# Performance work log

Hardware: AMD Instinct MI355X
Metric: run time of the kernel (lower is better)

Reference implementation:

```python
import jax, jax.numpy as jnp
import numpy as np

B, T, N, F = 16, 12, 1024, 8
H = 64        # hidden_size
K = 2         # diffusion order (DCRNN k == DiffConv gnn_kernel)
HORIZON = 12
E = 32 * N    # number of edges


def setup_inputs() -> dict:
    key = jax.random.key(0)
    ks = jax.random.split(key, 16)
    s = 0.05
    inp = {}
    inp['x'] = jax.random.normal(ks[0], (B, T, N, F), jnp.float32)
    inp['edge_index'] = jax.random.randint(ks[1], (2, E), 0, N)
    inp['edge_weight'] = jax.random.uniform(ks[2], (E,), jnp.float32)
    inp['adj'] = jax.random.uniform(ks[3], (N, N), jnp.float32)
    # encoder Linear(F -> H)
    inp['W_enc'] = jax.random.normal(ks[4], (F, H), jnp.float32) * s
    inp['b_enc'] = jnp.zeros((H,), jnp.float32)
    # NodeEmbedding(n_nodes, H)
    inp['node_emb'] = jax.random.normal(ks[5], (N, H), jnp.float32) * s
    # DCRNN gates: DenseGraphConvOrderK(2H -> H), 2 supports x K hops (include_self=False)
    gin = 2 * H * 2 * K
    inp['W_r'] = jax.random.normal(ks[6], (gin, H), jnp.float32) * s
    inp['b_r'] = jnp.zeros((H,), jnp.float32)
    inp['W_u'] = jax.random.normal(ks[7], (gin, H), jnp.float32) * s
    inp['b_u'] = jnp.zeros((H,), jnp.float32)
    inp['W_c'] = jax.random.normal(ks[8], (gin, H), jnp.float32) * s
    inp['b_c'] = jnp.zeros((H,), jnp.float32)
    # DiffConv filters: Linear(H*(2K+1) -> H), root_weight=True, add_backward=True
    din = H * (2 * K + 1)
    inp['W_diff'] = jax.random.normal(ks[9], (din, H), jnp.float32) * s
    inp['b_diff'] = jnp.zeros((H,), jnp.float32)
    # decoder Linear(H -> F*HORIZON)
    inp['W_dec'] = jax.random.normal(ks[10], (H, F * HORIZON), jnp.float32) * s
    inp['b_dec'] = jnp.zeros((F * HORIZON,), jnp.float32)
    return inp


def _dgconv(x, supports, W, b):
    # DenseGraphConvOrderK, include_self=False: for each support, K hop powers, concat on channels.
    feats = []
    for a in supports:  # a: [n, n], row-normalized transition matrix
        x1 = x
        for _ in range(K):
            x1 = jnp.einsum('bvc,wv->bwc', x1, a)
            feats.append(x1)
    return jnp.concatenate(feats, axis=-1) @ W + b


def _forward(x, edge_index, edge_weight, adj, W_enc, b_enc, node_emb,
             W_r, b_r, W_u, b_u, W_c, b_c, W_diff, b_diff, W_dec, b_dec):
    # --- DenseGraphConvOrderK.compute_support: fwd/bwd row-normalized transitions ---
    adj_fwd = adj / adj.sum(1, keepdims=True)
    adjT = adj.T
    adj_bwd = adjT / adjT.sum(1, keepdims=True)
    supports = (adj_fwd, adj_bwd)

    # encoder + node embeddings (broadcast over batch & time)
    x_enc = x @ W_enc + b_enc + node_emb  # [B, T, N, H]

    # --- DenseDCRNN: GRU with diffusion-conv gates, scan over time ---
    def step(h, xt):
        xh = jnp.concatenate([xt, h], axis=-1)                 # [B, N, 2H]
        r = jax.nn.sigmoid(_dgconv(xh, supports, W_r, b_r))    # forget/reset gate
        u = jax.nn.sigmoid(_dgconv(xh, supports, W_u, b_u))    # update gate
        xc = jnp.concatenate([xt, r * h], axis=-1)
        c = jnp.tanh(_dgconv(xc, supports, W_c, b_c))          # candidate
        h_new = u * h + (1.0 - u) * c
        return h_new, None

    h0 = jnp.zeros((B, N, H), x_enc.dtype)
    h, _ = jax.lax.scan(step, h0, jnp.swapaxes(x_enc, 0, 1))   # last state, [B, N, H]

    # --- DiffConv readout on sparse edge list (root + K fwd hops + K bwd hops) ---
    src, dst = edge_index[0], edge_index[1]

    def norm_w(group_idx):
        deg = jax.ops.segment_sum(edge_weight, group_idx, num_segments=N)
        inv = jnp.where(deg > 0, 1.0 / deg, 0.0)
        return edge_weight * inv[group_idx]

    w_fwd = norm_w(dst)  # normalize over target (dim=1)
    w_bwd = norm_w(src)  # flipped edges, normalized over their targets (= src)

    feats = [h]
    for s_, d_, w_ in ((src, dst, w_fwd), (dst, src, w_bwd)):
        xs = h
        for _ in range(K):
            msg = xs[:, s_, :] * w_[None, :, None]             # [B, E, H]
            xs = jnp.zeros_like(h).at[:, d_, :].add(msg)
            feats.append(xs)
    z = jnp.concatenate(feats, axis=-1) @ W_diff + b_diff      # [B, N, H]

    # decoder + rearrange 'b n (t f) -> b t n f'
    out = z @ W_dec + b_dec                                    # [B, N, HORIZON*F]
    return out.reshape(B, N, HORIZON, F).transpose(0, 2, 1, 3) # [B, HORIZON, N, F]


def reference(x, edge_index, edge_weight, adj, W_enc, b_enc, node_emb,
              W_r, b_r, W_u, b_u, W_c, b_c, W_diff, b_diff, W_dec, b_dec):
    return _forward(x, edge_index, edge_weight, adj, W_enc, b_enc, node_emb,
                    W_r, b_r, W_u, b_u, W_c, b_c, W_diff, b_diff, W_dec, b_dec)
```

## Files before the change

### kernel.cpp

```cpp
#include <hip/hip_runtime.h>
#include <math.h>

#define BB 16
#define TT 12
#define NN 1024
#define FF 8
#define HH 64
#define EE 32768
#define DIN 320
#define ODIM 96
#define APAD 40

typedef _Float16 v8h __attribute__((ext_vector_type(8)));
typedef float v4f __attribute__((ext_vector_type(4)));

__device__ __forceinline__ unsigned short f2h(float v) {
    _Float16 h = (_Float16)v;
    unsigned short u;
    __builtin_memcpy(&u, &h, 2);
    return u;
}
__device__ __forceinline__ float h2f(unsigned short u) {
    _Float16 h;
    __builtin_memcpy(&h, &u, 2);
    return (float)h;
}
__device__ __forceinline__ void gl_lds16(const void* g, void* l) {
    __builtin_amdgcn_global_load_lds(
        (const __attribute__((address_space(1))) unsigned int*)g,
        (__attribute__((address_space(3))) unsigned int*)l, 16, 0, 0);
}

__global__ void k_ei_detect(const int* __restrict__ ei_raw, int* __restrict__ flag) {
    __shared__ int s[256];
    s[threadIdx.x] = ei_raw[2 * threadIdx.x + 1];
    __syncthreads();
    for (int st = 128; st > 0; st >>= 1) {
        if (threadIdx.x < st) s[threadIdx.x] |= s[threadIdx.x + st];
        __syncthreads();
    }
    if (threadIdx.x == 0) flag[0] = (s[0] == 0) ? 1 : 0;
}
__global__ void k_ei_norm(const int* __restrict__ ei_raw, const int* __restrict__ flag,
                          int* __restrict__ ei32) {
    int j = blockIdx.x * 256 + threadIdx.x;
    ei32[j] = flag[0] ? ei_raw[2 * j] : ei_raw[j];
}

__global__ void k_rowsum(const float* __restrict__ adj, float* __restrict__ rinv) {
    __shared__ float s[256];
    int i = blockIdx.x;
    float acc = 0.f;
    for (int j = threadIdx.x; j < NN; j += 256) acc += adj[i * NN + j];
    s[threadIdx.x] = acc;
    __syncthreads();
    for (int st = 128; st > 0; st >>= 1) {
        if (threadIdx.x < st) s[threadIdx.x] += s[threadIdx.x + st];
        __syncthreads();
    }
    if (threadIdx.x == 0) rinv[i] = (s[0] != 0.f) ? 1.f / s[0] : 0.f;
}
__global__ void k_colsumP(const float* __restrict__ adj, float* __restrict__ csum) {
    int bi = blockIdx.x;
    int j4 = threadIdx.x * 4;
    float4 acc = {0.f, 0.f, 0.f, 0.f};
    const float* base = adj + (size_t)bi * 16 * NN + j4;
    #pragma unroll
    for (int r = 0; r < 16; r++) {
        float4 v = *(const float4*)(base + (size_t)r * NN);
        acc.x += v.x; acc.y += v.y; acc.z += v.z; acc.w += v.w;
    }
    atomicAdd(&csum[j4 + 0], acc.x);
    atomicAdd(&csum[j4 + 1], acc.y);
    atomicAdd(&csum[j4 + 2], acc.z);
    atomicAdd(&csum[j4 + 3], acc.w);
}
__global__ void k_cinv(const float* __restrict__ csum, float* __restrict__ cinv) {
    int j = blockIdx.x * 256 + threadIdx.x;
    float s = csum[j];
    cinv[j] = (s != 0.f) ? 1.f / s : 0.f;
}

__global__ __launch_bounds__(256) void k_prepA(
        const float* __restrict__ adj, const float* __restrict__ rinv,
        const float* __restrict__ cinv, unsigned short* __restrict__ Mp) {
    int w0 = blockIdx.x * 64, v0 = blockIdx.y * 64;
    __shared__ float T[64][68];
    int row = threadIdx.x >> 2, cs = (threadIdx.x & 3) * 16;
    #pragma unroll
    for (int j = 0; j < 4; j++)
        *(float4*)&T[row][cs + j * 4] = *(const float4*)(adj + (size_t)(w0 + row) * NN + v0 + cs + j * 4);
    __syncthreads();
    {
        float sc = rinv[w0 + row];
        unsigned short h8[16];
        #pragma unroll
        for (int j = 0; j < 16; j++) h8[j] = f2h(T[row][cs + j] * sc);
        size_t ofs = (size_t)(w0 + row) * NN + v0 + cs;
        ((uint4*)(Mp + ofs))[0] = *(uint4*)&h8[0];
        ((uint4*)(Mp + ofs))[1] = *(uint4*)&h8[8];
    }
    {
        float sc = cinv[v0 + row];
        unsigned short h8[16];
        #pragma unroll
        for (int j = 0; j < 16; j++) h8[j] = f2h(T[cs + j][row] * sc);
        size_t ofs = (size_t)2048 * NN + (size_t)(v0 + row) * NN + w0 + cs;
        ((uint4*)(Mp + ofs))[0] = *(uint4*)&h8[0];
        ((uint4*)(Mp + ofs))[1] = *(uint4*)&h8[8];
    }
}

__global__ __launch_bounds__(256) void k_msq(unsigned short* __restrict__ M) {
    int zz = blockIdx.z;
    size_t srcb = (size_t)zz * 2048 * NN;
    size_t dstb = srcb + (size_t)1024 * NN;
    int w0 = blockIdx.x * 64, n0 = blockIdx.y * 64;

    __shared__ unsigned short sA[64 * APAD];
    __shared__ unsigned short sB[64 * APAD];

    int tid = threadIdx.x;
    int lane = tid & 63, wave = tid >> 6;
    int wr = (wave >> 1) * 32, wc = (wave & 1) * 32;
    int l15 = lane & 15, quad = lane >> 4;
    int arow = tid >> 2, akk = (tid & 3) * 8;
    int bkr = tid & 31, bc8 = (tid >> 5) * 8;

    v4f acc[2][2];
    #pragma unroll
    for (int i = 0; i < 2; i++)
        #pragma unroll
        for (int j = 0; j < 2; j++) { acc[i][j][0]=0.f; acc[i][j][1]=0.f; acc[i][j][2]=0.f; acc[i][j][3]=0.f; }

    for (int k0 = 0; k0 < NN; k0 += 32) {
        *(uint4*)&sA[arow * APAD + akk] = *(const uint4*)(M + srcb + (size_t)(w0 + arow) * NN + k0 + akk);
        uint4 bh = *(const uint4*)(M + srcb + (size_t)(k0 + bkr) * NN + n0 + bc8);
        const unsigned short* ph = (const unsigned short*)&bh;
        #pragma unroll
        for (int j = 0; j < 8; j++) sB[(bc8 + j) * APAD + bkr] = ph[j];
        __syncthreads();

        v8h a0 = *(const v8h*)&sA[(wr + l15) * APAD + quad * 8];
        v8h a1 = *(const v8h*)&sA[(wr + 16 + l15) * APAD + quad * 8];
        #pragma unroll
        for (int j = 0; j < 2; j++) {
            v8h bb = *(const v8h*)&sB[(wc + j * 16 + l15) * APAD + quad * 8];
            acc[0][j] = __builtin_amdgcn_mfma_f32_16x16x32_f16(a0, bb, acc[0][j], 0, 0, 0);
            acc[1][j] = __builtin_amdgcn_mfma_f32_16x16x32_f16(a1, bb, acc[1][j], 0, 0, 0);
        }
        __syncthreads();
    }

    #pragma unroll
    for (int i = 0; i < 2; i++)
        #pragma unroll
        for (int j = 0; j < 2; j++) {
            int rb = w0 + wr + i * 16 + quad * 4;
            int cc = n0 + wc + j * 16 + l15;
            #pragma unroll
            for (int rr = 0; rr < 4; rr++)
                M[dstb + (size_t)(rb + rr) * NN + cc] = f2h(acc[i][j][rr]);
        }
}

__global__ void k_m2frag(const unsigned short* __restrict__ P, unsigned short* __restrict__ F) {
    size_t t = (size_t)blockIdx.x * 256 + threadIdx.x;
    int rowloc = (int)(t & 63);
    int kc = (int)((t >> 6) & 127);
    int T = (int)(t >> 13);
    size_t src = ((size_t)(T * 64 + rowloc) * NN) + kc * 8;
    *(uint4*)(F + t * 8) = *(const uint4*)(P + src);
}

__global__ void k_xT(const float* __restrict__ x, unsigned short* __restrict__ XallT) {
    int bx = blockIdx.x;
    int t = bx >> 4, b = bx & 15;
    int tid = threadIdx.x;
    int f = tid & 7, half = tid >> 3;
    const float* xs = x + ((size_t)b * TT + t) * NN * FF + f;
    int n0 = half * 32;
    unsigned short v[32];
    #pragma unroll
    for (int i = 0; i < 32; i++) v[i] = f2h(xs[(size_t)(n0 + i) * FF]);
    unsigned short* dst = XallT + ((size_t)bx * 8 + f) * NN + n0;
    #pragma unroll
    for (int i = 0; i < 4; i++) *(uint4*)(dst + i * 8) = *(uint4*)&v[i * 8];
}
__global__ void k_embT(const float* __restrict__ emb, unsigned short* __restrict__ XallT) {
    int c = blockIdx.x;
    int n0 = threadIdx.x * 4;
    unsigned short v[4];
    #pragma unroll
    for (int j = 0; j < 4; j++) v[j] = f2h(emb[(size_t)(n0 + j) * HH + c]);
    *(uint2*)(XallT + (size_t)(1536 + c) * NN + n0) = *(uint2*)v;
}

__global__ __launch_bounds__(512) void k_hopX(
        const unsigned short* __restrict__ Mf,
        const unsigned short* __restrict__ XallT,
        unsigned short* __restrict__ AX, unsigned short* __restrict__ Eg) {
    int bid = blockIdx.x;
    int rt = bid & 31;
    int y  = bid >> 5;
    int g = rt >> 3;
    int n0 = (rt & 7) * 128;
    int c0 = y * 128;

    __shared__ unsigned short sA[2][16 * 512];
    __shared__ unsigned short sX[2][16 * 512];

    int tid = threadIdx.x;
    int lane = tid & 63, wave = tid >> 6;
    int rh = wave >> 2, cq = wave & 3;
    int l15 = lane & 15, quad = lane >> 4;

    v4f acc[4][2];
    #pragma unroll
    for (int i = 0; i < 4; i++)
        #pragma unroll
        for (int j = 0; j < 2; j++) { acc[i][j][0]=0.f; acc[i][j][1]=0.f; acc[i][j][2]=0.f; acc[i][j][3]=0.f; }

    auto STAGE = [&](int buf, int k0) {
        #pragma unroll
        for (int s = 0; s < 4; s++) {
            int id = wave + s * 8;
            if (id < 16) {
                int ah = id >> 3, kh = (id >> 2) & 1, rf = id & 3;
                const unsigned short* src = Mf +
                    ((size_t)(rt * 2 + ah) * 8192 +
                     (size_t)((k0 >> 3) + kh * 4 + quad) * 64 + rf * 16 + l15) * 8;
                gl_lds16(src, &sA[buf][id * 512]);
            } else {
                int xi = id - 16, cj = xi >> 1, kh = xi & 1;
                const unsigned short* src = XallT +
                    (size_t)(c0 + cj * 16 + l15) * NN + k0 + kh * 32 + quad * 8;
                gl_lds16(src, &sX[buf][xi * 512]);
            }
        }
    };

    STAGE(0, 0);
    STAGE(1, 64);

    int lu = lane * 8;
    for (int kt = 0; kt < 16; kt++) {
        int cur = kt & 1;
        if (kt < 15) asm volatile("s_waitcnt vmcnt(4)" ::: "memory");
        else         asm volatile("s_waitcnt vmcnt(0)" ::: "memory");
        __builtin_amdgcn_s_barrier();
        asm volatile("" ::: "memory");
        #pragma unroll
        for (int kh = 0; kh < 2; kh++) {
            v8h a[4], bx[2];
            #pragma unroll
            for (int rf = 0; rf < 4; rf++)
                a[rf] = *(const v8h*)&sA[cur][(rh * 8 + kh * 4 + rf) * 512 + lu];
            #pragma unroll
            for (int j = 0; j < 2; j++)
                bx[j] = *(const v8h*)&sX[cur][((cq * 2 + j) * 2 + kh) * 512 + lu];
            #pragma unroll
            for (int rf = 0; rf < 4; rf++)
                #pragma unroll
                for (int j = 0; j < 2; j++)
                    acc[rf][j] = __builtin_amdgcn_mfma_f32_16x16x32_f16(a[rf], bx[j], acc[rf][j], 0, 0, 0);
        }
        asm volatile("" ::: "memory");
        __builtin_amdgcn_s_barrier();
        asm volatile("" ::: "memory");
        if (kt < 14) STAGE(cur, (kt + 2) * 64);
    }

    #pragma unroll
    for (int rf = 0; rf < 4; rf++)
        #pragma unroll
        for (int j = 0; j < 2; j++) {
            int col = c0 + cq * 32 + j * 16 + l15;
            #pragma unroll
            for (int rr = 0; rr < 4; rr++) {
                int nrow = n0 + rh * 64 + rf * 16 + quad * 4 + rr;
                if (col < 1536) {
                    int tb = col >> 3, f = col & 7;
                    AX[((size_t)tb * NN + nrow) * 32 + g * 8 + f] = f2h(acc[rf][j][rr]);
                } else if (col < 1600) {
                    int cc = col - 1536;
                    Eg[((size_t)(g << 10) + nrow) * 64 + cc] = f2h(acc[rf][j][rr]);
                }
            }
        }
}

__global__ void k_veg(const float* __restrict__ W_enc,
                      const float* __restrict__ W_r, const float* __restrict__ W_u,
                      const float* __restrict__ W_c, float* __restrict__ Veg) {
    int idx = blockIdx.x * 256 + threadIdx.x;
    int c = idx & 63;
    int gf = (idx >> 6) & 31;
    int G = idx >> 11;
    int g = gf >> 3, f = gf & 7;
    const float* W = (G == 0) ? W_r : ((G == 1) ? W_u : W_c);
    float acc = 0.f;
    for (int c2 = 0; c2 < 64; c2++)
        acc += W_enc[f * HH + c2] * W[(size_t)(g * 128 + c2) * HH + c];
    Veg[idx] = acc;
}

__global__ void k_constE(const unsigned short* __restrict__ Eg, const float* __restrict__ b_enc,
                         const float* __restrict__ W_r, const float* __restrict__ W_u,
                         const float* __restrict__ W_c, float* __restrict__ constE) {
    int G = blockIdx.y;
    int n = blockIdx.x * 4 + (threadIdx.x >> 6);
    int c = threadIdx.x & 63;
    const float* W = (G == 0) ? W_r : ((G == 1) ? W_u : W_c);
    float acc = 0.f;
    for (int g = 0; g < 4; g++)
        for (int c2 = 0; c2 < 64; c2++)
            acc += (h2f(Eg[((size_t)(g << 10) + n) * 64 + c2]) + b_enc[c2]) *
                   W[(size_t)(g * 128 + c2) * HH + c];
    constE[((size_t)G << 16) + (size_t)n * 64 + c] = acc;
}

__global__ void k_wfragH(const float* __restrict__ W_r, const float* __restrict__ W_u,
                         const float* __restrict__ W_c,
                         unsigned short* __restrict__ Fr, unsigned short* __restrict__ Fu,
                         unsigned short* __restrict__ Fc) {
    int idx = blockIdx.x * 256 + threadIdx.x;
    int G = idx >> 14;
    int r = idx & 16383;
    int e = r & 7, l = (r >> 3) & 63;
    int rest = r >> 9;
    int ks = rest & 7, cj = rest >> 3;
    int c = cj * 16 + (l & 15);
    int k = ks * 32 + (l >> 4) * 8 + e;
    int g = k >> 6, c2 = k & 63;
    const float* W = (G == 0) ? W_r : ((G == 1) ? W_u : W_c);
    unsigned short* F = (G == 0) ? Fr : ((G == 1) ? Fu : Fc);
    F[r] = f2h(W[(size_t)(g * 128 + 64 + c2) * HH + c]);
}
__global__ void k_wfragX(const float* __restrict__ Veg, unsigned short* __restrict__ Wx) {
    int idx = blockIdx.x * 256 + threadIdx.x;
    int G = idx >> 11;
    int r = idx & 2047;
    int e = r & 7, l = (r >> 3) & 63;
    int cj = r >> 9;
    int c = cj * 16 + (l & 15);
    int k = (l >> 4) * 8 + e;
    Wx[idx] = f2h(Veg[(size_t)G * 2048 + (size_t)k * 64 + c]);
}

__global__ void k_wfragO(const float* __restrict__ W_diff, const float* __restrict__ W_dec,
                         unsigned short* __restrict__ Wf) {
    int idx = blockIdx.x * 256 + threadIdx.x;
    int e = idx & 7, l = (idx >> 3) & 63;
    int rest = idx >> 9;
    int ks = rest % 10, cj = rest / 10;
    int o = cj * 16 + (l & 15);
    int k = ks * 32 + (l >> 4) * 8 + e;
    float acc = 0.f;
    for (int c = 0; c < 64; c++) acc += W_diff[(size_t)k * HH + c] * W_dec[(size_t)c * ODIM + o];
    Wf[idx] = f2h(acc);
}
__global__ void k_bzd(const float* __restrict__ b_diff, const float* __restrict__ W_dec,
                      const float* __restrict__ b_dec, float* __restrict__ bzd) {
    int o = threadIdx.x;
    float acc = b_dec[o];
    for (int c = 0; c < 64; c++) acc += b_diff[c] * W_dec[(size_t)c * ODIM + o];
    bzd[o] = acc;
}

__global__ __launch_bounds__(512) void k_hopRU(
        const unsigned short* __restrict__ Mf,
        const unsigned short* __restrict__ XhH,
        const unsigned short* __restrict__ AXt,
        const unsigned short* __restrict__ WfrH, const unsigned short* __restrict__ WfuH,
        const unsigned short* __restrict__ Wxr, const unsigned short* __restrict__ Wxu,
        const float* __restrict__ b_r, const float* __restrict__ b_u,
        const float* __restrict__ constE,
        const float* __restrict__ h,
        unsigned short* __restrict__ XhR, float* __restrict__ ubuf) {
    int bid = blockIdx.x;
    int b = bid >> 5, nth = bid & 31;
    int nt = nth >> 1, hb = nth & 1;
    int n0 = nth * 32;

    __shared__ unsigned short S[2][24 * 512];

    int tid = threadIdx.x;
    int lane = tid & 63, wave = tid >> 6;
    int l15 = lane & 15, quad = lane >> 4;
    int g = wave >> 1, rh = wave & 1;

    const unsigned short* Xbase = XhH + (size_t)b * 64 * NN;

    v4f acc[4];
    #pragma unroll
    for (int j = 0; j < 4; j++) { acc[j][0]=0.f; acc[j][1]=0.f; acc[j][2]=0.f; acc[j][3]=0.f; }

    auto STAGE = [&](int buf, int k0) {
        #pragma unroll
        for (int s = 0; s < 3; s++) {
            int id = wave + s * 8;
            if (id < 16) {
                int gg = id >> 2, kh = (id >> 1) & 1, rfi = id & 1;
                int rf = hb * 2 + rfi;
                const unsigned short* src = Mf +
                    ((size_t)(gg * 16 + nt) * 8192 +
                     (size_t)((k0 >> 3) + kh * 4 + quad) * 64 + rf * 16 + l15) * 8;
                gl_lds16(src, &S[buf][id * 512]);
            } else {
                int xi = id - 16, cj = xi >> 1, kh = xi & 1;
                const unsigned short* src = Xbase +
                    (size_t)(cj * 16 + l15) * NN + k0 + kh * 32 + quad * 8;
                gl_lds16(src, &S[buf][id * 512]);
            }
        }
    };

    STAGE(0, 0);
    STAGE(1, 64);

    int lu = lane * 8;
    for (int kt = 0; kt < 16; kt++) {
        int cur = kt & 1;
        if (kt < 15) asm volatile("s_waitcnt vmcnt(3)" ::: "memory");
        else         asm volatile("s_waitcnt vmcnt(0)" ::: "memory");
        __builtin_amdgcn_s_barrier();
        asm volatile("" ::: "memory");
        #pragma unroll
        for (int kh = 0; kh < 2; kh++) {
            v8h a = *(const v8h*)&S[cur][(g * 4 + kh * 2 + rh) * 512 + lu];
            #pragma unroll
            for (int cj = 0; cj < 4; cj++) {
                v8h bx = *(const v8h*)&S[cur][(16 + cj * 2 + kh) * 512 + lu];
                acc[cj] = __builtin_amdgcn_mfma_f32_16x16x32_f16(a, bx, acc[cj], 0, 0, 0);
            }
        }
        asm volatile("" ::: "memory");
        __builtin_amdgcn_s_barrier();
        asm volatile("" ::: "memory");
        if (kt < 14) STAGE(cur, (kt + 2) * 64);
    }

    unsigned short* Yt = &S[0][0];
    #pragma unroll
    for (int cj = 0; cj < 4; cj++) {
        int col = g * 64 + cj * 16 + l15;
        #pragma unroll
        for (int rr = 0; rr < 4; rr++) {
            int row = rh * 16 + quad * 4 + rr;
            Yt[row * 264 + col] = f2h(acc[cj][rr]);
        }
    }
    __syncthreads();

    int gate = wave >> 2, rw = (wave >> 1) & 1, ch = wave & 1;
    const unsigned short* WH = gate ? WfuH : WfrH;
    const unsigned short* WX = gate ? Wxu : Wxr;
    const float* bias = gate ? b_u : b_r;
    const float* cE = constE + ((size_t)gate << 16);

    v4f acc2[2];
    #pragma unroll
    for (int j = 0; j < 2; j++) { acc2[j][0]=0.f; acc2[j][1]=0.f; acc2[j][2]=0.f; acc2[j][3]=0.f; }

    {
        v8h ax = *(const v8h*)(AXt + ((size_t)(b << 10) + n0 + rw * 16 + l15) * 32 + quad * 8);
        #pragma unroll
        for (int j = 0; j < 2; j++) {
            v8h bf = *(const v8h*)(WX + (size_t)(ch * 2 + j) * 512 + lu);
            acc2[j] = __builtin_amdgcn_mfma_f32_16x16x32_f16(ax, bf, acc2[j], 0, 0, 0);
        }
    }
    #pragma unroll
    for (int ks = 0; ks < 8; ks++) {
        v8h a = *(const v8h*)&Yt[(rw * 16 + l15) * 264 + ks * 32 + quad * 8];
        #pragma unroll
        for (int j = 0; j < 2; j++) {
            v8h bf = *(const v8h*)(WH + (size_t)((ch * 2 + j) * 8 + ks) * 512 + lu);
            acc2[j] = __builtin_amdgcn_mfma_f32_16x16x32_f16(a, bf, acc2[j], 0, 0, 0);
        }
    }

    unsigned short* sT = &S[1][0];
    if (gate == 0) {
        #pragma unroll
        for (int j = 0; j < 2; j++) {
            int c = (ch * 2 + j) * 16 + l15;
            float bb = bias[c];
            #pragma unroll
            for (int rr = 0; rr < 4; rr++) {
                int nl = rw * 16 + quad * 4 + rr;
                size_t row = (size_t)(b << 10) + n0 + nl;
                float pre = acc2[j][rr] + bb + cE[(size_t)(n0 + nl) * 64 + c];
                float r = 1.f / (1.f + expf(-pre));
                sT[c * 36 + nl] = f2h(r * h[row * 64 + c]);
            }
        }
    } else {
        #pragma unroll
        for (int j = 0; j < 2; j++) {
            int c = (ch * 2 + j) * 16 + l15;
            float bb = bias[c];
            #pragma unroll
            for (int rr = 0; rr < 4; rr++) {
                int nl = rw * 16 + quad * 4 + rr;
                size_t row = (size_t)(b << 10) + n0 + nl;
                float pre = acc2[j][rr] + bb + cE[(size_t)(n0 + nl) * 64 + c];
                ubuf[row * 64 + c] = 1.f / (1.f + expf(-pre));
            }
        }
    }
    __syncthreads();
    {
        int c = tid >> 3, n4 = (tid & 7) * 4;
        *(uint2*)(XhR + ((size_t)b * 64 + c) * NN + n0 + n4) = *(uint2*)&sT[c * 36 + n4];
    }
}

__global__ __launch_bounds__(512) void k_hopC(
        const unsigned short* __restrict__ Mf,
        const unsigned short* __restrict__ XhR,
        const unsigned short* __restrict__ AXt,
        const unsigned short* __restrict__ WfcH, const unsigned short* __restrict__ Wxc,
        const float* __restrict__ b_c,
        const float* __restrict__ constE,
        const float* __restrict__ ubuf,
        float* __restrict__ h, unsigned short* __restrict__ XhH) {
    int bid = blockIdx.x;
    int b = bid >> 5, nth = bid & 31;
    int nt = nth >> 1, hb = nth & 1;
    int n0 = nth * 32;

    __shared__ unsigned short S[2][24 * 512];

    int tid = threadIdx.x;
    int lane = tid & 63, wave = tid >> 6;
    int l15 = lane & 15, quad = lane >> 4;
    int g = wave >> 1, rh = wave & 1;

    const unsigned short* Xbase = XhR + (size_t)b * 64 * NN;

    v4f acc[4];
    #pragma unroll
    for (int j = 0; j < 4; j++) { acc[j][0]=0.f; acc[j][1]=0.f; acc[j][2]=0.f; acc[j][3]=0.f; }

    auto STAGE = [&](int buf, int k0) {
        #pragma unroll
        for (int s = 0; s < 3; s++) {
            int id = wave + s * 8;
            if (id < 16) {
                int gg = id >> 2, kh = (id >> 1) & 1, rfi = id & 1;
                int rf = hb * 2 + rfi;
                const unsigned short* src = Mf +
                    ((size_t)(gg * 16 + nt) * 8192 +
                     (size_t)((k0 >> 3) + kh * 4 + quad) * 64 + rf * 16 + l15) * 8;
                gl_lds16(src, &S[buf][id * 512]);
            } else {
                int xi = id - 16, cj = xi >> 1, kh = xi & 1;
                const unsigned short* src = Xbase +
                    (size_t)(cj * 16 + l15) * NN + k0 + kh * 32 + quad * 8;
                gl_lds16(src, &S[buf][id * 512]);
            }
        }
    };

    STAGE(0, 0);
    STAGE(1, 64);

    int lu = lane * 8;
    for (int kt = 0; kt < 16; kt++) {
        int cur = kt & 1;
        if (kt < 15) asm volatile("s_waitcnt vmcnt(3)" ::: "memory");
        else         asm volatile("s_waitcnt vmcnt(0)" ::: "memory");
        __builtin_amdgcn_s_barrier();
        asm volatile("" ::: "memory");
        #pragma unroll
        for (int kh = 0; kh < 2; kh++) {
            v8h a = *(const v8h*)&S[cur][(g * 4 + kh * 2 + rh) * 512 + lu];
            #pragma unroll
            for (int cj = 0; cj < 4; cj++) {
                v8h bx = *(const v8h*)&S[cur][(16 + cj * 2 + kh) * 512 + lu];
                acc[cj] = __builtin_amdgcn_mfma_f32_16x16x32_f16(a, bx, acc[cj], 0, 0, 0);
            }
        }
        asm volatile("" ::: "memory");
        __builtin_amdgcn_s_barrier();
        asm volatile("" ::: "memory");
        if (kt < 14) STAGE(cur, (kt + 2) * 64);
    }

    unsigned short* Yt = &S[0][0];
    #pragma unroll
    for (int cj = 0; cj < 4; cj++) {
        int col = g * 64 + cj * 16 + l15;
        #pragma unroll
        for (int rr = 0; rr < 4; rr++) {
            int row = rh * 16 + quad * 4 + rr;
            Yt[row * 264 + col] = f2h(acc[cj][rr]);
        }
    }
    __syncthreads();

    int ch = wave >> 1, rw = wave & 1;
    const float* cE = constE + ((size_t)2 << 16);

    v4f acc2;
    acc2[0]=0.f; acc2[1]=0.f; acc2[2]=0.f; acc2[3]=0.f;

    {
        v8h ax = *(const v8h*)(AXt + ((size_t)(b << 10) + n0 + rw * 16 + l15) * 32 + quad * 8);
        v8h bf = *(const v8h*)(Wxc + (size_t)ch * 512 + lu);
        acc2 = __builtin_amdgcn_mfma_f32_16x16x32_f16(ax, bf, acc2, 0, 0, 0);
    }
    #pragma unroll
    for (int ks = 0; ks < 8; ks++) {
        v8h a = *(const v8h*)&Yt[(rw * 16 + l15) * 264 + ks * 32 + quad * 8];
        v8h bf = *(const v8h*)(WfcH + (size_t)(ch * 8 + ks) * 512 + lu);
        acc2 = __builtin_amdgcn_mfma_f32_16x16x32_f16(a, bf, acc2, 0, 0, 0);
    }

    unsigned short* sT = &S[1][0];
    {
        int c = ch * 16 + l15;
        float bb = b_c[c];
        #pragma unroll
        for (int rr = 0; rr < 4; rr++) {
            int nl = rw * 16 + quad * 4 + rr;
            size_t row = (size_t)(b << 10) + n0 + nl;
            float pre = acc2[rr] + bb + cE[(size_t)(n0 + nl) * 64 + c];
            float cv = tanhf(pre);
            float u = ubuf[row * 64 + c];
            float hv = h[row * 64 + c];
            float hn = u * hv + (1.f - u) * cv;
            h[row * 64 + c] = hn;
            sT[c * 36 + nl] = f2h(hn);
        }
    }
    __syncthreads();
    {
        int c = tid >> 3, n4 = (tid & 7) * 4;
        *(uint2*)(XhH + ((size_t)b * 64 + c) * NN + n0 + n4) = *(uint2*)&sT[c * 36 + n4];
    }
}

__global__ __launch_bounds__(512) void k_hopA(
        const unsigned short* __restrict__ Mf,
        const unsigned short* __restrict__ Xb,
        unsigned short* __restrict__ Yout, int out_stride, int out_gmul, int out_off) {
    int bid = blockIdx.x;
    int rt = bid & 31;
    int bp = bid >> 5;
    int g = rt >> 3;
    int n0 = (rt & 7) * 128;

    __shared__ unsigned short sA[2][16 * 512];
    __shared__ unsigned short sX[2][16 * 512];

    int tid = threadIdx.x;
    int lane = tid & 63, wave = tid >> 6;
    int rh = wave >> 2, cq = wave & 3;
    int l15 = lane & 15, quad = lane >> 4;

    const unsigned short* Xbase = Xb + (size_t)(bp * 2) * 64 * NN;

    v4f acc[4][2];
    #pragma unroll
    for (int i = 0; i < 4; i++)
        #pragma unroll
        for (int j = 0; j < 2; j++) { acc[i][j][0]=0.f; acc[i][j][1]=0.f; acc[i][j][2]=0.f; acc[i][j][3]=0.f; }

    auto STAGE = [&](int buf, int k0) {
        #pragma unroll
        for (int s = 0; s < 4; s++) {
            int id = wave + s * 8;
            if (id < 16) {
                int ah = id >> 3, kh = (id >> 2) & 1, rf = id & 3;
                const unsigned short* src = Mf +
                    ((size_t)(rt * 2 + ah) * 8192 +
                     (size_t)((k0 >> 3) + kh * 4 + quad) * 64 + rf * 16 + l15) * 8;
                gl_lds16(src, &sA[buf][id * 512]);
            } else {
                int xi = id - 16, cj = xi >> 1, kh = xi & 1;
                const unsigned short* src = Xbase +
                    (size_t)(cj * 16 + l15) * NN + k0 + kh * 32 + quad * 8;
                gl_lds16(src, &sX[buf][xi * 512]);
            }
        }
    };

    STAGE(0, 0);
    STAGE(1, 64);

    int lu = lane * 8;
    for (int kt = 0; kt < 16; kt++) {
        int cur = kt & 1;
        if (kt < 15) asm volatile("s_waitcnt vmcnt(4)" ::: "memory");
        else         asm volatile("s_waitcnt vmcnt(0)" ::: "memory");
        __builtin_amdgcn_s_barrier();
        asm volatile("" ::: "memory");
        #pragma unroll
        for (int kh = 0; kh < 2; kh++) {
            v8h a[4], bx[2];
            #pragma unroll
            for (int rf = 0; rf < 4; rf++)
                a[rf] = *(const v8h*)&sA[cur][(rh * 8 + kh * 4 + rf) * 512 + lu];
            #pragma unroll
            for (int j = 0; j < 2; j++)
                bx[j] = *(const v8h*)&sX[cur][((cq * 2 + j) * 2 + kh) * 512 + lu];
            #pragma unroll
            for (int rf = 0; rf < 4; rf++)
                #pragma unroll
                for (int j = 0; j < 2; j++)
                    acc[rf][j] = __builtin_amdgcn_mfma_f32_16x16x32_f16(a[rf], bx[j], acc[rf][j], 0, 0, 0);
        }
        asm volatile("" ::: "memory");
        __builtin_amdgcn_s_barrier();
        asm volatile("" ::: "memory");
        if (kt < 14) STAGE(cur, (kt + 2) * 64);
    }

    #pragma unroll
    for (int rf = 0; rf < 4; rf++)
        #pragma unroll
        for (int j = 0; j < 2; j++) {
            int colloc = cq * 32 + j * 16 + l15;
            int b = bp * 2 + (colloc >> 6);
            int c = colloc & 63;
            unsigned short* Y = Yout + (size_t)b * NN * out_stride + out_gmul * g + out_off + c;
            int rbase = n0 + rh * 64 + rf * 16 + quad * 4;
            #pragma unroll
            for (int rr = 0; rr < 4; rr++)
                Y[(size_t)(rbase + rr) * out_stride] = f2h(acc[rf][j][rr]);
        }
}

__global__ __launch_bounds__(256) void k_out(
        const unsigned short* __restrict__ featd,
        const unsigned short* __restrict__ Wf_o, const float* __restrict__ bzd,
        float* __restrict__ out) {
    int row0 = blockIdx.x * 64;
    int tid = threadIdx.x, lane = tid & 63, wave = tid >> 6;
    int l15 = lane & 15, quad = lane >> 4;

    v4f acc[6];
    #pragma unroll
    for (int cj = 0; cj < 6; cj++) { acc[cj][0]=0.f; acc[cj][1]=0.f; acc[cj][2]=0.f; acc[cj][3]=0.f; }

    const unsigned short* fbase = featd + (size_t)(row0 + wave * 16 + l15) * DIN + quad * 8;
    #pragma unroll 2
    for (int ks = 0; ks < 10; ks++) {
        v8h a = *(const v8h*)(fbase + ks * 32);
        #pragma unroll
        for (int cj = 0; cj < 6; cj++) {
            v8h bf = *(const v8h*)(Wf_o + (size_t)(cj * 10 + ks) * 512 + lane * 8);
            acc[cj] = __builtin_amdgcn_mfma_f32_16x16x32_f16(a, bf, acc[cj], 0, 0, 0);
        }
    }
    #pragma unroll
    for (int cj = 0; cj < 6; cj++) {
        int o = cj * 16 + l15;
        int t = o >> 3, f = o & 7;
        float bb = bzd[o];
        #pragma unroll
        for (int rr = 0; rr < 4; rr++) {
            int row = row0 + wave * 16 + quad * 4 + rr;
            int b = row >> 10, n = row & 1023;
            out[(((size_t)b * TT + t) * NN + n) * FF + f] = acc[cj][rr] + bb;
        }
    }
}

__global__ void k_deg(const int* __restrict__ ei32, const float* __restrict__ ew,
                      float* __restrict__ degd, float* __restrict__ degs) {
    int e = blockIdx.x * 256 + threadIdx.x;
    float w = ew[e];
    atomicAdd(&degd[ei32[EE + e]], w);
    atomicAdd(&degs[ei32[e]], w);
}
__global__ void k_spadd(const int* __restrict__ ei32, const float* __restrict__ ew,
                        const float* __restrict__ degd, const float* __restrict__ degs,
                        float* __restrict__ temp) {
    int e = blockIdx.x * 256 + threadIdx.x;
    int s = ei32[e], d = ei32[EE + e];
    float w = ew[e];
    float dd = degd[d], ds = degs[s];
    float wfv = dd > 0.f ? w / dd : 0.f;
    float wbv = ds > 0.f ? w / ds : 0.f;
    atomicAdd(&temp[(size_t)d * NN + s], wfv);
    atomicAdd(&temp[(size_t)NN * NN + (size_t)s * NN + d], wbv);
}
__global__ void k_spconv(const float* __restrict__ temp, unsigned short* __restrict__ Mp) {
    size_t i0 = ((size_t)blockIdx.x * 256 + threadIdx.x) * 8;
    size_t dst = (i0 < (size_t)NN * NN) ? i0 : i0 + (size_t)NN * NN;
    unsigned short h8[8];
    #pragma unroll
    for (int j = 0; j < 8; j++) h8[j] = f2h(temp[i0 + j]);
    *(uint4*)(Mp + dst) = *(uint4*)h8;
}

__global__ void k_featd_h(const float* __restrict__ h, unsigned short* __restrict__ featd) {
    size_t idx = (size_t)blockIdx.x * 256 + threadIdx.x;
    size_t row = idx >> 6; int c = (int)(idx & 63);
    featd[row * DIN + c] = f2h(h[idx]);
}

extern "C" void kernel_launch(void* const* d_in, const int* in_sizes, int n_in,
                              void* d_out, int out_size, void* d_ws, size_t ws_size,
                              hipStream_t stream) {
    const float* x      = (const float*)d_in[0];
    const int*   eiraw  = (const int*)  d_in[1];
    const float* ew     = (const float*)d_in[2];
    const float* adj    = (const float*)d_in[3];
    const float* W_enc  = (const float*)d_in[4];
    const float* b_enc  = (const float*)d_in[5];
    const float* emb    = (const float*)d_in[6];
    const float* W_r    = (const float*)d_in[7];
    const float* b_r    = (const float*)d_in[8];
    const float* W_u    = (const float*)d_in[9];
    const float* b_u    = (const float*)d_in[10];
    const float* W_c    = (const float*)d_in[11];
    const float* b_c    = (const float*)d_in[12];
    const float* W_diff = (const float*)d_in[13];
    const float* b_diff = (const float*)d_in[14];
    const float* W_dec  = (const float*)d_in[15];
    const float* b_dec  = (const float*)d_in[16];

    unsigned short* Mf    = (unsigned short*)d_ws;
    unsigned short* XhH   = Mf + (size_t)4096 * NN;
    unsigned short* XhR   = XhH + (size_t)BB * 64 * NN;
    unsigned short* featd = XhR + (size_t)BB * 64 * NN;
    float* h    = (float*)(featd + (size_t)BB * NN * DIN);
    float* ubuf = h + (size_t)BB * NN * HH;
    unsigned short* AXall = (unsigned short*)(ubuf + (size_t)BB * NN * HH);
    unsigned short* Mp    = AXall;
    unsigned short* XallT = AXall + (size_t)192 * NN * 32;
    unsigned short* Eg    = XallT + (size_t)1600 * NN;
    float* sptmp  = (float*)(Eg + (size_t)4 * NN * 64);
    float* constE = sptmp + (size_t)2 * NN * NN;
    float* Veg    = constE + (size_t)3 * NN * 64;
    unsigned short* WfH  = (unsigned short*)(Veg + 3 * 32 * 64);
    unsigned short* WfrH = WfH;
    unsigned short* WfuH = WfH + 16384;
    unsigned short* WfcH = WfH + 32768;
    unsigned short* Wx   = WfH + 49152;
    unsigned short* Wf_o = Wx + 6144;
    float* bzd  = (float*)(Wf_o + 30720);
    float* rinv = bzd + ODIM;
    float* cinv = rinv + NN;
    int*   eifl = (int*)(cinv + NN);
    int*   ei32 = eifl + 4;
    float* degd = (float*)(ei32 + 2 * EE);
    float* degs = degd + NN;
    float* csum = degs + NN;

    hipMemsetAsync(h, 0, (size_t)BB * NN * HH * 4, stream);
    hipMemsetAsync(XhH, 0, (size_t)BB * 64 * NN * 2, stream);
    hipMemsetAsync(csum, 0, NN * 4, stream);

    k_rowsum<<<NN, 256, 0, stream>>>(adj, rinv);
    k_colsumP<<<64, 256, 0, stream>>>(adj, csum);
    k_cinv<<<NN / 256, 256, 0, stream>>>(csum, cinv);
    k_prepA<<<dim3(16, 16), 256, 0, stream>>>(adj, rinv, cinv, Mp);
    k_msq<<<dim3(16, 16, 2), 256, 0, stream>>>(Mp);
    k_m2frag<<<2048, 256, 0, stream>>>(Mp, Mf);

    k_xT<<<TT * BB, 256, 0, stream>>>(x, XallT);
    k_embT<<<64, 256, 0, stream>>>(emb, XallT);
    k_hopX<<<13 * 32, 512, 0, stream>>>(Mf, XallT, AXall, Eg);
    k_veg<<<24, 256, 0, stream>>>(W_enc, W_r, W_u, W_c, Veg);
    k_constE<<<dim3(256, 3), 256, 0, stream>>>(Eg, b_enc, W_r, W_u, W_c, constE);
    k_wfragH<<<192, 256, 0, stream>>>(W_r, W_u, W_c, WfrH, WfuH, WfcH);
    k_wfragX<<<24, 256, 0, stream>>>(Veg, Wx);
    k_wfragO<<<120, 256, 0, stream>>>(W_diff, W_dec, Wf_o);
    k_bzd<<<1, ODIM, 0, stream>>>(b_diff, W_dec, b_dec, bzd);

    for (int t = 0; t < TT; t++) {
        const unsigned short* AXt = AXall + (size_t)t * BB * NN * 32;
        k_hopRU<<<512, 512, 0, stream>>>(Mf, XhH, AXt, WfrH, WfuH, Wx, Wx + 2048,
                                         b_r, b_u, constE, h, XhR, ubuf);
        k_hopC<<<512, 512, 0, stream>>>(Mf, XhR, AXt, WfcH, Wx + 4096,
                                        b_c, constE, ubuf, h, XhH);
    }

    k_ei_detect<<<1, 256, 0, stream>>>(eiraw, eifl);
    k_ei_norm<<<2 * EE / 256, 256, 0, stream>>>(eiraw, eifl, ei32);
    hipMemsetAsync(degd, 0, (size_t)2 * NN * 4, stream);
    hipMemsetAsync(sptmp, 0, (size_t)2 * NN * NN * 4, stream);
    k_deg<<<EE / 256, 256, 0, stream>>>(ei32, ew, degd, degs);
    k_spadd<<<EE / 256, 256, 0, stream>>>(ei32, ew, degd, degs, sptmp);
    k_spconv<<<2 * NN * NN / (256 * 8), 256, 0, stream>>>(sptmp, Mp);
    k_msq<<<dim3(16, 16, 2), 256, 0, stream>>>(Mp);
    k_m2frag<<<2048, 256, 0, stream>>>(Mp, Mf);
    k_featd_h<<<BB * NN * HH / 256, 256, 0, stream>>>(h, featd);
    k_hopA<<<8 * 32, 512, 0, stream>>>(Mf, XhH, featd, DIN, 64, 64);
    k_out<<<BB * NN / 64, 256, 0, stream>>>(featd, Wf_o, bzd, (float*)d_out);
}
```

Measured before the change: 722.1 us.

## Triple-buffer hop kernels and retile adjacency squaring with pre-transposed operand

The recurrent hop kernels move from double to triple LDS buffering, issuing the next stage's async loads right after the barrier and dropping the second barrier per k-step. The adjacency-squaring GEMM is replaced by a transpose kernel plus a 128x128-tile MFMA kernel that stages both operands with direct global-to-LDS loads in a double-buffered pipeline. This aims to hide memory latency and cut barrier stalls, at the cost of more LDS per block (possibly lower occupancy) and an extra transpose pass through scratch memory.

```diff
diff --git a/kernel.cpp b/kernel.cpp
--- a/kernel.cpp
+++ b/kernel.cpp
@@ -9,7 +9,6 @@
 #define EE 32768
 #define DIN 320
 #define ODIM 96
-#define APAD 40
 
 typedef _Float16 v8h __attribute__((ext_vector_type(8)));
 typedef float v4f __attribute__((ext_vector_type(4)));
@@ -111,56 +110,104 @@
     }
 }
 
-__global__ __launch_bounds__(256) void k_msq(unsigned short* __restrict__ M) {
+__global__ __launch_bounds__(256) void k_mT(const unsigned short* __restrict__ Mp,
+                                            unsigned short* __restrict__ Mt) {
     int zz = blockIdx.z;
-    size_t srcb = (size_t)zz * 2048 * NN;
-    size_t dstb = srcb + (size_t)1024 * NN;
-    int w0 = blockIdx.x * 64, n0 = blockIdx.y * 64;
-
-    __shared__ unsigned short sA[64 * APAD];
-    __shared__ unsigned short sB[64 * APAD];
+    int r0 = blockIdx.x * 64, c0 = blockIdx.y * 64;
+    __shared__ unsigned short T[64][72];
+    int row = threadIdx.x >> 2, cs = (threadIdx.x & 3) * 16;
+    const unsigned short* src = Mp + (size_t)zz * 2048 * NN + (size_t)(r0 + row) * NN + c0 + cs;
+    *(uint4*)&T[row][cs] = *(const uint4*)src;
+    *(uint4*)&T[row][cs + 8] = *(const uint4*)(src + 8);
+    __syncthreads();
+    unsigned short v[16];
+    #pragma unroll
+    for (int j = 0; j < 16; j++) v[j] = T[cs + j][row];
+    unsigned short* dst = Mt + (size_t)zz * 1024 * NN + (size_t)(c0 + row) * NN + r0 + cs;
+    *(uint4*)dst = *(uint4*)&v[0];
+    *(uint4*)(dst + 8) = *(uint4*)&v[8];
+}
+
+__global__ __launch_bounds__(512) void k_msq2(unsigned short* __restrict__ M,
+                                              const unsigned short* __restrict__ Mt) {
+    int bid = blockIdx.x;
+    int zz = bid >> 6, t = bid & 63;
+    int r0 = (t >> 3) * 128, c0 = (t & 7) * 128;
+    size_t asec = (size_t)zz * 2048 * NN;
+    const unsigned short* Arows = M + asec;
+    const unsigned short* Brows = Mt + (size_t)zz * 1024 * NN;
+    unsigned short* D = M + asec + (size_t)1024 * NN;
+
+    __shared__ unsigned short sA[2][16 * 512];
+    __shared__ unsigned short sB[2][16 * 512];
 
     int tid = threadIdx.x;
     int lane = tid & 63, wave = tid >> 6;
-    int wr = (wave >> 1) * 32, wc = (wave & 1) * 32;
+    int rh = wave >> 2, cq = wave & 3;
     int l15 = lane & 15, quad = lane >> 4;
-    int arow = tid >> 2, akk = (tid & 3) * 8;
-    int bkr = tid & 31, bc8 = (tid >> 5) * 8;
-
-    v4f acc[2][2];
-    #pragma unroll
-    for (int i = 0; i < 2; i++)
+
+    v4f acc[4][2];
+    #pragma unroll
+    for (int i = 0; i < 4; i++)
         #pragma unroll
         for (int j = 0; j < 2; j++) { acc[i][j][0]=0.f; acc[i][j][1]=0.f; acc[i][j][2]=0.f; acc[i][j][3]=0.f; }
 
-    for (int k0 = 0; k0 < NN; k0 += 32) {
-        *(uint4*)&sA[arow * APAD + akk] = *(const uint4*)(M + srcb + (size_t)(w0 + arow) * NN + k0 + akk);
-        uint4 bh = *(const uint4*)(M + srcb + (size_t)(k0 + bkr) * NN + n0 + bc8);
-        const unsigned short* ph = (const unsigned short*)&bh;
-        #pragma unroll
-        for (int j = 0; j < 8; j++) sB[(bc8 + j) * APAD + bkr] = ph[j];
-        __syncthreads();
-
-        v8h a0 = *(const v8h*)&sA[(wr + l15) * APAD + quad * 8];
-        v8h a1 = *(const v8h*)&sA[(wr + 16 + l15) * APAD + quad * 8];
+    auto STAGE = [&](int buf, int k0) {
+        #pragma unroll
+        for (int s = 0; s < 4; s++) {
+            int id = wave + s * 8;
+            if (id < 16) {
+                int rf = id >> 1, kh = id & 1;
+                const unsigned short* src = Arows + (size_t)(r0 + rf * 16 + l15) * NN + k0 + kh * 32 + quad * 8;
+                gl_lds16(src, &sA[buf][id * 512]);
+            } else {
+                int xi = id - 16, cj = xi >> 1, kh = xi & 1;
+                const unsigned short* src = Brows + (size_t)(c0 + cj * 16 + l15) * NN + k0 + kh * 32 + quad * 8;
+                gl_lds16(src, &sB[buf][xi * 512]);
+            }
+        }
+    };
+
+    STAGE(0, 0);
+    STAGE(1, 64);
+
+    int lu = lane * 8;
+    for (int kt = 0; kt < 16; kt++) {
+        int cur = kt & 1;
+        if (kt < 15) asm volatile("s_waitcnt vmcnt(4)" ::: "memory");
+        else         asm volatile("s_waitcnt vmcnt(0)" ::: "memory");
+        __builtin_amdgcn_s_barrier();
+        asm volatile("" ::: "memory");
+        #pragma unroll
+        for (int kh = 0; kh < 2; kh++) {
+            v8h a[4], bx[2];
+            #pragma unroll
+            for (int i = 0; i < 4; i++)
+                a[i] = *(const v8h*)&sA[cur][((rh * 4 + i) * 2 + kh) * 512 + lu];
+            #pragma unroll
+            for (int j = 0; j < 2; j++)
+                bx[j] = *(const v8h*)&sB[cur][((cq * 2 + j) * 2 + kh) * 512 + lu];
+            #pragma unroll
+            for (int i = 0; i < 4; i++)
+                #pragma unroll
+                for (int j = 0; j < 2; j++)
+                    acc[i][j] = __builtin_amdgcn_mfma_f32_16x16x32_f16(a[i], bx[j], acc[i][j], 0, 0, 0);
+        }
+        asm volatile("" ::: "memory");
+        __builtin_amdgcn_s_barrier();
+        asm volatile("" ::: "memory");
+        if (kt < 14) STAGE(cur, (kt + 2) * 64);
+    }
+
+    #pragma unroll
+    for (int rf = 0; rf < 4; rf++)
         #pragma unroll
         for (int j = 0; j < 2; j++) {
-            v8h bb = *(const v8h*)&sB[(wc + j * 16 + l15) * APAD + quad * 8];
-            acc[0][j] = __builtin_amdgcn_mfma_f32_16x16x32_f16(a0, bb, acc[0][j], 0, 0, 0);
-            acc[1][j] = __builtin_amdgcn_mfma_f32_16x16x32_f16(a1, bb, acc[1][j], 0, 0, 0);
-        }
-        __syncthreads();
-    }
-
-    #pragma unroll
-    for (int i = 0; i < 2; i++)
-        #pragma unroll
-        for (int j = 0; j < 2; j++) {
-            int rb = w0 + wr + i * 16 + quad * 4;
-            int cc = n0 + wc + j * 16 + l15;
+            int row = r0 + rh * 64 + rf * 16 + quad * 4;
+            int col = c0 + cq * 32 + j * 16 + l15;
             #pragma unroll
             for (int rr = 0; rr < 4; rr++)
-                M[dstb + (size_t)(rb + rr) * NN + cc] = f2h(acc[i][j][rr]);
+                D[(size_t)(row + rr) * NN + col] = f2h(acc[rf][j][rr]);
         }
 }
 
@@ -383,7 +430,7 @@
     int nt = nth >> 1, hb = nth & 1;
     int n0 = nth * 32;
 
-    __shared__ unsigned short S[2][24 * 512];
+    __shared__ unsigned short S[3][24 * 512];
 
     int tid = threadIdx.x;
     int lane = tid & 63, wave = tid >> 6;
@@ -421,11 +468,12 @@
 
     int lu = lane * 8;
     for (int kt = 0; kt < 16; kt++) {
-        int cur = kt & 1;
+        int cur = kt % 3;
         if (kt < 15) asm volatile("s_waitcnt vmcnt(3)" ::: "memory");
         else         asm volatile("s_waitcnt vmcnt(0)" ::: "memory");
         __builtin_amdgcn_s_barrier();
         asm volatile("" ::: "memory");
+        if (kt < 14) STAGE((kt + 2) % 3, (kt + 2) * 64);
         #pragma unroll
         for (int kh = 0; kh < 2; kh++) {
             v8h a = *(const v8h*)&S[cur][(g * 4 + kh * 2 + rh) * 512 + lu];
@@ -436,10 +484,8 @@
             }
         }
         asm volatile("" ::: "memory");
-        __builtin_amdgcn_s_barrier();
-        asm volatile("" ::: "memory");
-        if (kt < 14) STAGE(cur, (kt + 2) * 64);
-    }
+    }
+    __syncthreads();
 
     unsigned short* Yt = &S[0][0];
     #pragma unroll
@@ -531,7 +577,7 @@
     int nt = nth >> 1, hb = nth & 1;
     int n0 = nth * 32;
 
-    __shared__ unsigned short S[2][24 * 512];
+    __shared__ unsigned short S[3][24 * 512];
 
     int tid = threadIdx.x;
     int lane = tid & 63, wave = tid >> 6;
@@ -569,11 +615,12 @@
 
     int lu = lane * 8;
     for (int kt = 0; kt < 16; kt++) {
-        int cur = kt & 1;
+        int cur = kt % 3;
         if (kt < 15) asm volatile("s_waitcnt vmcnt(3)" ::: "memory");
         else         asm volatile("s_waitcnt vmcnt(0)" ::: "memory");
         __builtin_amdgcn_s_barrier();
         asm volatile("" ::: "memory");
+        if (kt < 14) STAGE((kt + 2) % 3, (kt + 2) * 64);
         #pragma unroll
         for (int kh = 0; kh < 2; kh++) {
             v8h a = *(const v8h*)&S[cur][(g * 4 + kh * 2 + rh) * 512 + lu];
@@ -584,10 +631,8 @@
             }
         }
         asm volatile("" ::: "memory");
-        __builtin_amdgcn_s_barrier();
-        asm volatile("" ::: "memory");
-        if (kt < 14) STAGE(cur, (kt + 2) * 64);
-    }
+    }
+    __syncthreads();
 
     unsigned short* Yt = &S[0][0];
     #pragma unroll
@@ -836,6 +881,7 @@
     unsigned short* XallT = AXall + (size_t)192 * NN * 32;
     unsigned short* Eg    = XallT + (size_t)1600 * NN;
     float* sptmp  = (float*)(Eg + (size_t)4 * NN * 64);
+    unsigned short* Mt = (unsigned short*)sptmp;
     float* constE = sptmp + (size_t)2 * NN * NN;
     float* Veg    = constE + (size_t)3 * NN * 64;
     unsigned short* WfH  = (unsigned short*)(Veg + 3 * 32 * 64);
@@ -861,7 +907,8 @@
     k_colsumP<<<64, 256, 0, stream>>>(adj, csum);
     k_cinv<<<NN / 256, 256, 0, stream>>>(csum, cinv);
     k_prepA<<<dim3(16, 16), 256, 0, stream>>>(adj, rinv, cinv, Mp);
-    k_msq<<<dim3(16, 16, 2), 256, 0, stream>>>(Mp);
+    k_mT<<<dim3(16, 16, 2), 256, 0, stream>>>(Mp, Mt);
+    k_msq2<<<128, 512, 0, stream>>>(Mp, Mt);
     k_m2frag<<<2048, 256, 0, stream>>>(Mp, Mf);
 
     k_xT<<<TT * BB, 256, 0, stream>>>(x, XallT);
@@ -889,7 +936,8 @@
     k_deg<<<EE / 256, 256, 0, stream>>>(ei32, ew, degd, degs);
     k_spadd<<<EE / 256, 256, 0, stream>>>(ei32, ew, degd, degs, sptmp);
     k_spconv<<<2 * NN * NN / (256 * 8), 256, 0, stream>>>(sptmp, Mp);
-    k_msq<<<dim3(16, 16, 2), 256, 0, stream>>>(Mp);
+    k_mT<<<dim3(16, 16, 2), 256, 0, stream>>>(Mp, Mt);
+    k_msq2<<<128, 512, 0, stream>>>(Mp, Mt);
     k_m2frag<<<2048, 256, 0, stream>>>(Mp, Mf);
     k_featd_h<<<BB * NN * HH / 256, 256, 0, stream>>>(h, featd);
     k_hopA<<<8 * 32, 512, 0, stream>>>(Mf, XhH, featd, DIN, 64, 64);
```

After: 724.4 us. No clear change (+0.3%).
